# Kernel tuning notes

Measured on AMD Instinct MI355X. Metric: run time of the kernel, lower is better.

The kernel has to match this reference:

```python
import jax, jax.numpy as jnp
import numpy as np

NEG_SLOPE = 0.2


def _gather_neighbour(pc, idx):
    # pc: (B, N, d), idx: (B, N, k) -> (B, N, k, d)
    B, N, d = pc.shape
    k = idx.shape[-1]
    flat = idx.reshape(B, N * k)[..., None]            # (B, N*k, 1)
    g = jnp.take_along_axis(pc, flat, axis=1)          # (B, N*k, d)
    return g.reshape(B, N, k, d)


def _block(x, idx, W2, g2, b2, W1, g1, b1):
    # gather -> 1x1 conv (BN folded, ReLU) -> max/mean over k -> concat -> 1x1 conv (BN folded, no act)
    g = _gather_neighbour(x, idx)                      # (B, N, k, d)
    h = jax.nn.relu(jnp.einsum('bnkd,de->bnke', g, W2) * g2 + b2)
    mx = h.max(axis=2)                                 # (B, N, d_out)
    mn = h.mean(axis=2)                                # (B, N, d_out)
    cat = jnp.concatenate([mx, mn], axis=-1)           # (B, N, 2*d_out)
    return jnp.einsum('bnc,cd->bnd', cat, W1) * g1 + b1


def setup_inputs() -> dict:
    key = jax.random.key(0)
    ks = jax.random.split(key, 8)
    B, N, K, D = 2, 65536, 16, 32
    x = jax.random.normal(ks[0], (B, N, D), dtype=jnp.float32)
    idx = jax.random.randint(ks[1], (B, N, K), 0, N, dtype=jnp.int32)
    L = 4  # four stacked blocks
    W2d = jax.random.normal(ks[2], (L, D, D), dtype=jnp.float32) * 0.05
    gamma2 = jnp.ones((L, 1, 1, 1, D), dtype=jnp.float32)
    beta2 = jax.random.normal(ks[3], (L, 1, 1, 1, D), dtype=jnp.float32) * 0.01
    W1d = jax.random.normal(ks[4], (L, 2 * D, D), dtype=jnp.float32) * 0.05
    gamma1 = jnp.ones((L, 1, 1, D), dtype=jnp.float32)
    beta1 = jax.random.normal(ks[5], (L, 1, 1, D), dtype=jnp.float32) * 0.01
    return {"x": x, "idx": idx, "W2d": W2d, "gamma2": gamma2, "beta2": beta2,
            "W1d": W1d, "gamma1": gamma1, "beta1": beta1}


def reference(x, idx, W2d, gamma2, beta2, W1d, gamma1, beta1):
    lrelu = lambda v: jax.nn.leaky_relu(v, NEG_SLOPE)
    blk = lambda inp, i: _block(inp, idx, W2d[i], gamma2[i][0], beta2[i][0],
                                W1d[i], gamma1[i][0], beta1[i][0])
    x1 = blk(x, 0)
    tmp = lrelu(x1)
    x2 = blk(tmp, 1)
    tmp = lrelu(x2 + x1)
    x3 = blk(tmp, 2)
    tmp = lrelu(x3 + x2)
    x4 = blk(tmp, 3)
    return lrelu(x1 + x2 + x3 + x4)
```

## Files before the change

### kernel.cpp

```cpp
#include <hip/hip_runtime.h>
#include <hip/hip_fp16.h>

namespace {

typedef _Float16 half8 __attribute__((ext_vector_type(8)));
typedef float f32x4 __attribute__((ext_vector_type(4)));

constexpr int kN = 65536;
constexpr int kD = 32;
constexpr int kPts = 2 * kN;
constexpr int kThreads = 256;
constexpr int kPtsPerWave = 16;
constexpr int kPtsPerBlk = 64;
constexpr int kBlocks = kPts / kPtsPerBlk;
static_assert(kBlocks * kPtsPerBlk == kPts, "grid must tile points exactly");
static_assert(kN % kPtsPerBlk == 0, "blocks must not straddle batch boundary");

__device__ __forceinline__ float relu_(float v) { return fmaxf(v, 0.f); }
__device__ __forceinline__ float lrelu_(float v) { return v >= 0.f ? v : 0.2f * v; }

__device__ __forceinline__ half8 load_bfrag(const float* __restrict__ W,
                                            int krow0, int ncol, int q)
{
    half8 b;
#pragma unroll
    for (int j = 0; j < 8; ++j)
        b[j] = (_Float16)W[(krow0 + q * 8 + j) * kD + ncol];
    return b;
}

__global__ __launch_bounds__(kThreads, 4)
void zprep_kernel(const float* __restrict__ x, const float* __restrict__ W2,
                  const float* __restrict__ g2v, const float* __restrict__ b2v,
                  __half* __restrict__ z)
{
    const int tid  = threadIdx.x;
    const int w    = tid >> 6;
    const int lane = tid & 63;
    const int n    = lane & 15;
    const int q    = lane >> 4;
    const int pbase = blockIdx.x * kPtsPerBlk + w * kPtsPerWave;
    const int point = pbase + n;

    const float4 x0 = reinterpret_cast<const float4*>(x)[point * 8 + q * 2];
    const float4 x1 = reinterpret_cast<const float4*>(x)[point * 8 + q * 2 + 1];
    half8 ax;
    ax[0] = (_Float16)x0.x; ax[1] = (_Float16)x0.y;
    ax[2] = (_Float16)x0.z; ax[3] = (_Float16)x0.w;
    ax[4] = (_Float16)x1.x; ax[5] = (_Float16)x1.y;
    ax[6] = (_Float16)x1.z; ax[7] = (_Float16)x1.w;

    const half8 b0 = load_bfrag(W2, 0, n, q);
    const half8 b1 = load_bfrag(W2, 0, 16 + n, q);
    f32x4 acc0 = {0.f, 0.f, 0.f, 0.f}, acc1 = {0.f, 0.f, 0.f, 0.f};
    acc0 = __builtin_amdgcn_mfma_f32_16x16x32_f16(ax, b0, acc0, 0, 0, 0);
    acc1 = __builtin_amdgcn_mfma_f32_16x16x32_f16(ax, b1, acc1, 0, 0, 0);

    const float g20 = g2v[n], g21 = g2v[16 + n];
    const float c20 = b2v[n], c21 = b2v[16 + n];
#pragma unroll
    for (int r = 0; r < 4; ++r) {
        const int pm = pbase + q * 4 + r;
        z[pm * kD + n]      = __float2half(relu_(fmaf(acc0[r], g20, c20)));
        z[pm * kD + 16 + n] = __float2half(relu_(fmaf(acc1[r], g21, c21)));
    }
}

template <int MODE>
__global__ __launch_bounds__(kThreads, 4)
void blk_kernel(const uint4* __restrict__ zsrc, const int4* __restrict__ idx,
                const float* __restrict__ W1, const float* __restrict__ g1v,
                const float* __restrict__ b1v,
                const float* __restrict__ W2n, const float* __restrict__ g2v,
                const float* __restrict__ b2v,
                const __half* __restrict__ prev, __half* __restrict__ cur,
                float* __restrict__ sacc, __half* __restrict__ znext)
{
    __shared__ __align__(16) _Float16 tb[4][16][40];

    const int tid  = threadIdx.x;
    const int w    = tid >> 6;
    const int lane = tid & 63;
    const int n    = lane & 15;
    const int q    = lane >> 4;
    const int pbase = blockIdx.x * kPtsPerBlk + w * kPtsPerWave;
    const int point = pbase + n;
    const int base  = point & ~(kN - 1);

    const int4 i0 = idx[point * 4 + 0];
    const int4 i1 = idx[point * 4 + 1];
    const int4 i2 = idx[point * 4 + 2];
    const int4 i3 = idx[point * 4 + 3];

    const half8 bA0 = load_bfrag(W1, 0, n, q);
    const half8 bA1 = load_bfrag(W1, 0, 16 + n, q);
    const half8 bB0 = load_bfrag(W1, 32, n, q);
    const half8 bB1 = load_bfrag(W1, 32, 16 + n, q);

    int rows[16];
    rows[0] = i0.x; rows[1] = i0.y; rows[2]  = i0.z; rows[3]  = i0.w;
    rows[4] = i1.x; rows[5] = i1.y; rows[6]  = i1.z; rows[7]  = i1.w;
    rows[8] = i2.x; rows[9] = i2.y; rows[10] = i2.z; rows[11] = i2.w;
    rows[12] = i3.x; rows[13] = i3.y; rows[14] = i3.z; rows[15] = i3.w;

    float mx[8], sm[8];
#pragma unroll
    for (int c = 0; c < 8; ++c) { mx[c] = 0.f; sm[c] = 0.f; }
#pragma unroll
    for (int k = 0; k < 16; ++k) {
        const uint4 u = zsrc[(base + rows[k]) * 4 + q];
        const __half2* h = reinterpret_cast<const __half2*>(&u);
#pragma unroll
        for (int c = 0; c < 4; ++c) {
            const float2 f = __half22float2(h[c]);
            mx[2 * c]     = fmaxf(mx[2 * c], f.x);     sm[2 * c]     += f.x;
            mx[2 * c + 1] = fmaxf(mx[2 * c + 1], f.y); sm[2 * c + 1] += f.y;
        }
    }
    half8 amax, amean;
#pragma unroll
    for (int c = 0; c < 8; ++c) {
        amax[c]  = (_Float16)mx[c];
        amean[c] = (_Float16)(sm[c] * 0.0625f);
    }

    f32x4 acc0 = {0.f, 0.f, 0.f, 0.f}, acc1 = {0.f, 0.f, 0.f, 0.f};
    acc0 = __builtin_amdgcn_mfma_f32_16x16x32_f16(amax,  bA0, acc0, 0, 0, 0);
    acc0 = __builtin_amdgcn_mfma_f32_16x16x32_f16(amean, bB0, acc0, 0, 0, 0);
    acc1 = __builtin_amdgcn_mfma_f32_16x16x32_f16(amax,  bA1, acc1, 0, 0, 0);
    acc1 = __builtin_amdgcn_mfma_f32_16x16x32_f16(amean, bB1, acc1, 0, 0, 0);

    const float g10 = g1v[n], g11 = g1v[16 + n];
    const float c10 = b1v[n], c11 = b1v[16 + n];

    float t0[4], t1[4];
#pragma unroll
    for (int r = 0; r < 4; ++r) {
        const int pm = pbase + q * 4 + r;
        const int o0 = pm * kD + n;
        const int o1 = o0 + 16;
        const float y0 = fmaf(acc0[r], g10, c10);
        const float y1 = fmaf(acc1[r], g11, c11);
        if (MODE == 0) {
            sacc[o0] = y0; sacc[o1] = y1;
            cur[o0] = __float2half(y0); cur[o1] = __float2half(y1);
            t0[r] = lrelu_(y0); t1[r] = lrelu_(y1);
        } else if (MODE == 1 || MODE == 2) {
            sacc[o0] += y0; sacc[o1] += y1;
            const float pv0 = __half2float(prev[o0]);
            const float pv1 = __half2float(prev[o1]);
            t0[r] = lrelu_(y0 + pv0); t1[r] = lrelu_(y1 + pv1);
            if (MODE == 1) { cur[o0] = __float2half(y0); cur[o1] = __float2half(y1); }
        } else {
            sacc[o0] = lrelu_(sacc[o0] + y0);
            sacc[o1] = lrelu_(sacc[o1] + y1);
        }
    }
    if (MODE == 3) return;

#pragma unroll
    for (int r = 0; r < 4; ++r) {
        tb[w][q * 4 + r][n]      = (_Float16)t0[r];
        tb[w][q * 4 + r][16 + n] = (_Float16)t1[r];
    }
    __syncthreads();
    const half8 at = *reinterpret_cast<const half8*>(&tb[w][n][q * 8]);

    const half8 bz0 = load_bfrag(W2n, 0, n, q);
    const half8 bz1 = load_bfrag(W2n, 0, 16 + n, q);
    f32x4 az0 = {0.f, 0.f, 0.f, 0.f}, az1 = {0.f, 0.f, 0.f, 0.f};
    az0 = __builtin_amdgcn_mfma_f32_16x16x32_f16(at, bz0, az0, 0, 0, 0);
    az1 = __builtin_amdgcn_mfma_f32_16x16x32_f16(at, bz1, az1, 0, 0, 0);

    const float g20 = g2v[n], g21 = g2v[16 + n];
    const float c20 = b2v[n], c21 = b2v[16 + n];
#pragma unroll
    for (int r = 0; r < 4; ++r) {
        const int pm = pbase + q * 4 + r;
        znext[pm * kD + n]      = __float2half(relu_(fmaf(az0[r], g20, c20)));
        znext[pm * kD + 16 + n] = __float2half(relu_(fmaf(az1[r], g21, c21)));
    }
}

}

extern "C" void kernel_launch(void* const* d_in, const int* in_sizes, int n_in,
                              void* d_out, int out_size, void* d_ws, size_t ws_size,
                              hipStream_t stream)
{
    const float* x   = (const float*)d_in[0];
    const int4*  idx = (const int4*)d_in[1];
    const float* W2d = (const float*)d_in[2];
    const float* g2  = (const float*)d_in[3];
    const float* b2  = (const float*)d_in[4];
    const float* W1d = (const float*)d_in[5];
    const float* g1  = (const float*)d_in[6];
    const float* b1  = (const float*)d_in[7];
    float* out = (float*)d_out;
    char*  ws  = (char*)d_ws;

    constexpr size_t kHalfMap = (size_t)kPts * kD * sizeof(__half);
    __half* zA = (__half*)(ws);
    __half* zB = (__half*)(ws + kHalfMap);
    __half* cA = (__half*)(ws + 2 * kHalfMap);
    __half* cB = (__half*)(ws + 3 * kHalfMap);

    const dim3 grid(kBlocks), blk(kThreads);
    zprep_kernel<<<grid, blk, 0, stream>>>(x, W2d, g2, b2, zA);
    blk_kernel<0><<<grid, blk, 0, stream>>>((const uint4*)zA, idx, W1d, g1, b1,
        W2d + 1 * kD * kD, g2 + 1 * kD, b2 + 1 * kD, nullptr, cA, out, zB);
    blk_kernel<1><<<grid, blk, 0, stream>>>((const uint4*)zB, idx,
        W1d + 1 * 2 * kD * kD, g1 + 1 * kD, b1 + 1 * kD,
        W2d + 2 * kD * kD, g2 + 2 * kD, b2 + 2 * kD, cA, cB, out, zA);
    blk_kernel<2><<<grid, blk, 0, stream>>>((const uint4*)zA, idx,
        W1d + 2 * 2 * kD * kD, g1 + 2 * kD, b1 + 2 * kD,
        W2d + 3 * kD * kD, g2 + 3 * kD, b2 + 3 * kD, cB, nullptr, out, zB);
    blk_kernel<3><<<grid, blk, 0, stream>>>((const uint4*)zB, idx,
        W1d + 3 * 2 * kD * kD, g1 + 3 * kD, b1 + 3 * kD,
        nullptr, nullptr, nullptr, nullptr, nullptr, out, nullptr);
}
```

Measured before the change: 190.1 us.

## Pack weights into MFMA fragments, compress indices to 16-bit, permute channel layout

Adds a one-block pack kernel that converts all weight matrices into ready-made fp16 MFMA B-fragments, so the per-block scalar strided weight loads and conversions go away. zprep now also rewrites the int32 neighbour indices as 16-bit pairs, which halves index traffic in the three later gather kernels that read them. The z and cur maps use an interleaved channel permutation (half2 pairs of channels c and c+16), with the weight rows permuted to match. The epilogue goes through a wave-local LDS transpose with a wave barrier instead of __syncthreads, so sacc, prev and cur are accessed as wide float4/uint4 per point. In exchange there is an extra launch and workspace, and the 16-bit indices rely on N ≤ 65536.

```diff
diff --git a/kernel.cpp b/kernel.cpp
--- a/kernel.cpp
+++ b/kernel.cpp
@@ -10,36 +10,73 @@
 constexpr int kD = 32;
 constexpr int kPts = 2 * kN;
 constexpr int kThreads = 256;
-constexpr int kPtsPerWave = 16;
 constexpr int kPtsPerBlk = 64;
 constexpr int kBlocks = kPts / kPtsPerBlk;
+constexpr int kNumFrags = 24;
 static_assert(kBlocks * kPtsPerBlk == kPts, "grid must tile points exactly");
 static_assert(kN % kPtsPerBlk == 0, "blocks must not straddle batch boundary");
 
 __device__ __forceinline__ float relu_(float v) { return fmaxf(v, 0.f); }
 __device__ __forceinline__ float lrelu_(float v) { return v >= 0.f ? v : 0.2f * v; }
 
-__device__ __forceinline__ half8 load_bfrag(const float* __restrict__ W,
-                                            int krow0, int ncol, int q)
-{
-    half8 b;
-#pragma unroll
-    for (int j = 0; j < 8; ++j)
-        b[j] = (_Float16)W[(krow0 + q * 8 + j) * kD + ncol];
-    return b;
+__device__ __forceinline__ int pi_(int k) {
+    const int c = ((k >> 3) << 2) + ((k & 7) >> 1);
+    return (k & 1) ? c + 16 : c;
+}
+
+__global__ __launch_bounds__(kThreads)
+void pack_kernel(const float* __restrict__ W2d, const float* __restrict__ W1d,
+                 uint4* __restrict__ wpack)
+{
+    for (int id = threadIdx.x; id < kNumFrags * 64; id += kThreads) {
+        const int fid = id >> 6, l = id & 63, n = l & 15, q = l >> 4;
+        half8 v;
+        if (fid < 2) {
+            const int h = fid;
+#pragma unroll
+            for (int j = 0; j < 8; ++j)
+                v[j] = (_Float16)W2d[(q * 8 + j) * kD + h * 16 + n];
+        } else {
+            const int rel = fid - 2;
+            const int layer = (rel < 18) ? rel / 6 : 3;
+            const int sub   = (rel < 18) ? rel % 6 : rel - 18;
+            if (sub < 4) {
+                const int p = sub >> 1, h = sub & 1;
+#pragma unroll
+                for (int j = 0; j < 8; ++j)
+                    v[j] = (_Float16)W1d[layer * 2048 + (p * 32 + pi_(q * 8 + j)) * kD + h * 16 + n];
+            } else {
+                const int h = sub - 4;
+#pragma unroll
+                for (int j = 0; j < 8; ++j)
+                    v[j] = (_Float16)W2d[(layer + 1) * 1024 + pi_(q * 8 + j) * kD + h * 16 + n];
+            }
+        }
+        wpack[id] = *reinterpret_cast<const uint4*>(&v);
+    }
 }
 
 __global__ __launch_bounds__(kThreads, 4)
-void zprep_kernel(const float* __restrict__ x, const float* __restrict__ W2,
+void zprep_kernel(const float* __restrict__ x, const int4* __restrict__ idx4,
+                  const uint4* __restrict__ wfrag,
                   const float* __restrict__ g2v, const float* __restrict__ b2v,
-                  __half* __restrict__ z)
+                  __half2* __restrict__ z, uint2* __restrict__ idx16)
 {
     const int tid  = threadIdx.x;
+    {
+        const int p = blockIdx.x * kPtsPerBlk + (tid >> 2);
+        const int part = tid & 3;
+        const int4 iv = idx4[p * 4 + part];
+        uint2 o;
+        o.x = (unsigned)(iv.x & 0xFFFF) | ((unsigned)iv.y << 16);
+        o.y = (unsigned)(iv.z & 0xFFFF) | ((unsigned)iv.w << 16);
+        idx16[p * 4 + part] = o;
+    }
     const int w    = tid >> 6;
     const int lane = tid & 63;
     const int n    = lane & 15;
     const int q    = lane >> 4;
-    const int pbase = blockIdx.x * kPtsPerBlk + w * kPtsPerWave;
+    const int pbase = blockIdx.x * kPtsPerBlk + w * 16;
     const int point = pbase + n;
 
     const float4 x0 = reinterpret_cast<const float4*>(x)[point * 8 + q * 2];
@@ -50,65 +87,67 @@
     ax[4] = (_Float16)x1.x; ax[5] = (_Float16)x1.y;
     ax[6] = (_Float16)x1.z; ax[7] = (_Float16)x1.w;
 
-    const half8 b0 = load_bfrag(W2, 0, n, q);
-    const half8 b1 = load_bfrag(W2, 0, 16 + n, q);
-    f32x4 acc0 = {0.f, 0.f, 0.f, 0.f}, acc1 = {0.f, 0.f, 0.f, 0.f};
-    acc0 = __builtin_amdgcn_mfma_f32_16x16x32_f16(ax, b0, acc0, 0, 0, 0);
-    acc1 = __builtin_amdgcn_mfma_f32_16x16x32_f16(ax, b1, acc1, 0, 0, 0);
+    const uint4 u0 = wfrag[0 * 64 + lane];
+    const uint4 u1 = wfrag[1 * 64 + lane];
+    const half8 b0 = *reinterpret_cast<const half8*>(&u0);
+    const half8 b1 = *reinterpret_cast<const half8*>(&u1);
+    f32x4 a0 = {0.f, 0.f, 0.f, 0.f}, a1 = {0.f, 0.f, 0.f, 0.f};
+    a0 = __builtin_amdgcn_mfma_f32_16x16x32_f16(ax, b0, a0, 0, 0, 0);
+    a1 = __builtin_amdgcn_mfma_f32_16x16x32_f16(ax, b1, a1, 0, 0, 0);
 
     const float g20 = g2v[n], g21 = g2v[16 + n];
     const float c20 = b2v[n], c21 = b2v[16 + n];
 #pragma unroll
     for (int r = 0; r < 4; ++r) {
         const int pm = pbase + q * 4 + r;
-        z[pm * kD + n]      = __float2half(relu_(fmaf(acc0[r], g20, c20)));
-        z[pm * kD + 16 + n] = __float2half(relu_(fmaf(acc1[r], g21, c21)));
+        z[pm * 16 + n] = __floats2half2_rn(relu_(fmaf(a0[r], g20, c20)),
+                                           relu_(fmaf(a1[r], g21, c21)));
     }
 }
 
 template <int MODE>
 __global__ __launch_bounds__(kThreads, 4)
-void blk_kernel(const uint4* __restrict__ zsrc, const int4* __restrict__ idx,
-                const float* __restrict__ W1, const float* __restrict__ g1v,
-                const float* __restrict__ b1v,
-                const float* __restrict__ W2n, const float* __restrict__ g2v,
-                const float* __restrict__ b2v,
-                const __half* __restrict__ prev, __half* __restrict__ cur,
-                float* __restrict__ sacc, __half* __restrict__ znext)
-{
-    __shared__ __align__(16) _Float16 tb[4][16][40];
+void blk_kernel(const uint4* __restrict__ zsrc, const uint4* __restrict__ idx16,
+                const uint4* __restrict__ wfrag,
+                const float* __restrict__ g1v, const float* __restrict__ b1v,
+                const float* __restrict__ g2v, const float* __restrict__ b2v,
+                const uint4* __restrict__ prev, uint4* __restrict__ cur,
+                float* __restrict__ sacc, __half2* __restrict__ znext)
+{
+    __shared__ float2 tb[4][16][17];
 
     const int tid  = threadIdx.x;
     const int w    = tid >> 6;
     const int lane = tid & 63;
     const int n    = lane & 15;
     const int q    = lane >> 4;
-    const int pbase = blockIdx.x * kPtsPerBlk + w * kPtsPerWave;
+    const int pbase = blockIdx.x * kPtsPerBlk + w * 16;
     const int point = pbase + n;
-    const int base  = point & ~(kN - 1);
-
-    const int4 i0 = idx[point * 4 + 0];
-    const int4 i1 = idx[point * 4 + 1];
-    const int4 i2 = idx[point * 4 + 2];
-    const int4 i3 = idx[point * 4 + 3];
-
-    const half8 bA0 = load_bfrag(W1, 0, n, q);
-    const half8 bA1 = load_bfrag(W1, 0, 16 + n, q);
-    const half8 bB0 = load_bfrag(W1, 32, n, q);
-    const half8 bB1 = load_bfrag(W1, 32, 16 + n, q);
-
-    int rows[16];
-    rows[0] = i0.x; rows[1] = i0.y; rows[2]  = i0.z; rows[3]  = i0.w;
-    rows[4] = i1.x; rows[5] = i1.y; rows[6]  = i1.z; rows[7]  = i1.w;
-    rows[8] = i2.x; rows[9] = i2.y; rows[10] = i2.z; rows[11] = i2.w;
-    rows[12] = i3.x; rows[13] = i3.y; rows[14] = i3.z; rows[15] = i3.w;
+    const int base  = pbase & ~(kN - 1);
+
+    const uint4 iv0 = idx16[point * 2 + 0];
+    const uint4 iv1 = idx16[point * 2 + 1];
+
+    const uint4 f0 = wfrag[0 * 64 + lane];
+    const uint4 f1 = wfrag[1 * 64 + lane];
+    const uint4 f2 = wfrag[2 * 64 + lane];
+    const uint4 f3 = wfrag[3 * 64 + lane];
+    const half8 bA0 = *reinterpret_cast<const half8*>(&f0);
+    const half8 bA1 = *reinterpret_cast<const half8*>(&f1);
+    const half8 bB0 = *reinterpret_cast<const half8*>(&f2);
+    const half8 bB1 = *reinterpret_cast<const half8*>(&f3);
 
     float mx[8], sm[8];
 #pragma unroll
     for (int c = 0; c < 8; ++c) { mx[c] = 0.f; sm[c] = 0.f; }
+    const unsigned* ivw = reinterpret_cast<const unsigned*>(&iv0);
 #pragma unroll
     for (int k = 0; k < 16; ++k) {
-        const uint4 u = zsrc[(base + rows[k]) * 4 + q];
+        unsigned word;
+        if (k < 8) word = reinterpret_cast<const unsigned*>(&iv0)[k >> 1];
+        else       word = reinterpret_cast<const unsigned*>(&iv1)[(k - 8) >> 1];
+        const int row = (k & 1) ? (int)(word >> 16) : (int)(word & 0xFFFFu);
+        const uint4 u = zsrc[(base + row) * 4 + q];
         const __half2* h = reinterpret_cast<const __half2*>(&u);
 #pragma unroll
         for (int c = 0; c < 4; ++c) {
@@ -117,6 +156,7 @@
             mx[2 * c + 1] = fmaxf(mx[2 * c + 1], f.y); sm[2 * c + 1] += f.y;
         }
     }
+    (void)ivw;
     half8 amax, amean;
 #pragma unroll
     for (int c = 0; c < 8; ++c) {
@@ -132,42 +172,71 @@
 
     const float g10 = g1v[n], g11 = g1v[16 + n];
     const float c10 = b1v[n], c11 = b1v[16 + n];
-
-    float t0[4], t1[4];
 #pragma unroll
     for (int r = 0; r < 4; ++r) {
-        const int pm = pbase + q * 4 + r;
-        const int o0 = pm * kD + n;
-        const int o1 = o0 + 16;
-        const float y0 = fmaf(acc0[r], g10, c10);
-        const float y1 = fmaf(acc1[r], g11, c11);
-        if (MODE == 0) {
-            sacc[o0] = y0; sacc[o1] = y1;
-            cur[o0] = __float2half(y0); cur[o1] = __float2half(y1);
-            t0[r] = lrelu_(y0); t1[r] = lrelu_(y1);
-        } else if (MODE == 1 || MODE == 2) {
-            sacc[o0] += y0; sacc[o1] += y1;
-            const float pv0 = __half2float(prev[o0]);
-            const float pv1 = __half2float(prev[o1]);
-            t0[r] = lrelu_(y0 + pv0); t1[r] = lrelu_(y1 + pv1);
-            if (MODE == 1) { cur[o0] = __float2half(y0); cur[o1] = __float2half(y1); }
-        } else {
-            sacc[o0] = lrelu_(sacc[o0] + y0);
-            sacc[o1] = lrelu_(sacc[o1] + y1);
-        }
-    }
-    if (MODE == 3) return;
-
-#pragma unroll
-    for (int r = 0; r < 4; ++r) {
-        tb[w][q * 4 + r][n]      = (_Float16)t0[r];
-        tb[w][q * 4 + r][16 + n] = (_Float16)t1[r];
-    }
-    __syncthreads();
-    const half8 at = *reinterpret_cast<const half8*>(&tb[w][n][q * 8]);
-
-    const half8 bz0 = load_bfrag(W2n, 0, n, q);
-    const half8 bz1 = load_bfrag(W2n, 0, 16 + n, q);
+        tb[w][q * 4 + r][n] = make_float2(fmaf(acc0[r], g10, c10),
+                                          fmaf(acc1[r], g11, c11));
+    }
+    __builtin_amdgcn_wave_barrier();
+    float y8[8];
+#pragma unroll
+    for (int s = 0; s < 4; ++s) {
+        const float2 f = tb[w][n][q * 4 + s];
+        y8[2 * s] = f.x; y8[2 * s + 1] = f.y;
+    }
+
+    const int sb0 = point * kD + q * 4;
+    const int sb1 = sb0 + 16;
+    float t8[8];
+    if (MODE == 0) {
+        reinterpret_cast<float4*>(sacc)[sb0 >> 2] = make_float4(y8[0], y8[2], y8[4], y8[6]);
+        reinterpret_cast<float4*>(sacc)[sb1 >> 2] = make_float4(y8[1], y8[3], y8[5], y8[7]);
+        half8 ch;
+#pragma unroll
+        for (int c = 0; c < 8; ++c) ch[c] = (_Float16)y8[c];
+        cur[point * 4 + q] = *reinterpret_cast<const uint4*>(&ch);
+#pragma unroll
+        for (int c = 0; c < 8; ++c) t8[c] = lrelu_(y8[c]);
+    } else if (MODE == 1 || MODE == 2) {
+        float4 s0 = reinterpret_cast<const float4*>(sacc)[sb0 >> 2];
+        float4 s1 = reinterpret_cast<const float4*>(sacc)[sb1 >> 2];
+        s0.x += y8[0]; s0.y += y8[2]; s0.z += y8[4]; s0.w += y8[6];
+        s1.x += y8[1]; s1.y += y8[3]; s1.z += y8[5]; s1.w += y8[7];
+        reinterpret_cast<float4*>(sacc)[sb0 >> 2] = s0;
+        reinterpret_cast<float4*>(sacc)[sb1 >> 2] = s1;
+        const uint4 pv = prev[point * 4 + q];
+        const __half2* ph = reinterpret_cast<const __half2*>(&pv);
+#pragma unroll
+        for (int c = 0; c < 4; ++c) {
+            const float2 f = __half22float2(ph[c]);
+            t8[2 * c]     = lrelu_(y8[2 * c] + f.x);
+            t8[2 * c + 1] = lrelu_(y8[2 * c + 1] + f.y);
+        }
+        if (MODE == 1) {
+            half8 ch;
+#pragma unroll
+            for (int c = 0; c < 8; ++c) ch[c] = (_Float16)y8[c];
+            cur[point * 4 + q] = *reinterpret_cast<const uint4*>(&ch);
+        }
+    } else {
+        const float4 s0 = reinterpret_cast<const float4*>(sacc)[sb0 >> 2];
+        const float4 s1 = reinterpret_cast<const float4*>(sacc)[sb1 >> 2];
+        reinterpret_cast<float4*>(sacc)[sb0 >> 2] =
+            make_float4(lrelu_(s0.x + y8[0]), lrelu_(s0.y + y8[2]),
+                        lrelu_(s0.z + y8[4]), lrelu_(s0.w + y8[6]));
+        reinterpret_cast<float4*>(sacc)[sb1 >> 2] =
+            make_float4(lrelu_(s1.x + y8[1]), lrelu_(s1.y + y8[3]),
+                        lrelu_(s1.z + y8[5]), lrelu_(s1.w + y8[7]));
+        return;
+    }
+
+    half8 at;
+#pragma unroll
+    for (int c = 0; c < 8; ++c) at[c] = (_Float16)t8[c];
+    const uint4 f4 = wfrag[4 * 64 + lane];
+    const uint4 f5 = wfrag[5 * 64 + lane];
+    const half8 bz0 = *reinterpret_cast<const half8*>(&f4);
+    const half8 bz1 = *reinterpret_cast<const half8*>(&f5);
     f32x4 az0 = {0.f, 0.f, 0.f, 0.f}, az1 = {0.f, 0.f, 0.f, 0.f};
     az0 = __builtin_amdgcn_mfma_f32_16x16x32_f16(at, bz0, az0, 0, 0, 0);
     az1 = __builtin_amdgcn_mfma_f32_16x16x32_f16(at, bz1, az1, 0, 0, 0);
@@ -177,8 +246,8 @@
 #pragma unroll
     for (int r = 0; r < 4; ++r) {
         const int pm = pbase + q * 4 + r;
-        znext[pm * kD + n]      = __float2half(relu_(fmaf(az0[r], g20, c20)));
-        znext[pm * kD + 16 + n] = __float2half(relu_(fmaf(az1[r], g21, c21)));
+        znext[pm * 16 + n] = __floats2half2_rn(relu_(fmaf(az0[r], g20, c20)),
+                                               relu_(fmaf(az1[r], g21, c21)));
     }
 }
 
@@ -200,22 +269,28 @@
     char*  ws  = (char*)d_ws;
 
     constexpr size_t kHalfMap = (size_t)kPts * kD * sizeof(__half);
-    __half* zA = (__half*)(ws);
-    __half* zB = (__half*)(ws + kHalfMap);
-    __half* cA = (__half*)(ws + 2 * kHalfMap);
-    __half* cB = (__half*)(ws + 3 * kHalfMap);
+    __half2* zA = (__half2*)(ws);
+    __half2* zB = (__half2*)(ws + kHalfMap);
+    uint4*   cA = (uint4*)(ws + 2 * kHalfMap);
+    uint4*   cB = (uint4*)(ws + 3 * kHalfMap);
+    uint2*   idx16 = (uint2*)(ws + 4 * kHalfMap);
+    uint4*   wpack = (uint4*)(ws + 4 * kHalfMap + (size_t)kPts * 32);
 
     const dim3 grid(kBlocks), blk(kThreads);
-    zprep_kernel<<<grid, blk, 0, stream>>>(x, W2d, g2, b2, zA);
-    blk_kernel<0><<<grid, blk, 0, stream>>>((const uint4*)zA, idx, W1d, g1, b1,
-        W2d + 1 * kD * kD, g2 + 1 * kD, b2 + 1 * kD, nullptr, cA, out, zB);
-    blk_kernel<1><<<grid, blk, 0, stream>>>((const uint4*)zB, idx,
-        W1d + 1 * 2 * kD * kD, g1 + 1 * kD, b1 + 1 * kD,
-        W2d + 2 * kD * kD, g2 + 2 * kD, b2 + 2 * kD, cA, cB, out, zA);
-    blk_kernel<2><<<grid, blk, 0, stream>>>((const uint4*)zA, idx,
-        W1d + 2 * 2 * kD * kD, g1 + 2 * kD, b1 + 2 * kD,
-        W2d + 3 * kD * kD, g2 + 3 * kD, b2 + 3 * kD, cB, nullptr, out, zB);
-    blk_kernel<3><<<grid, blk, 0, stream>>>((const uint4*)zB, idx,
-        W1d + 3 * 2 * kD * kD, g1 + 3 * kD, b1 + 3 * kD,
-        nullptr, nullptr, nullptr, nullptr, nullptr, out, nullptr);
-}
+    pack_kernel<<<dim3(1), blk, 0, stream>>>(W2d, W1d, wpack);
+    zprep_kernel<<<grid, blk, 0, stream>>>(x, idx, wpack, g2, b2, zA, idx16);
+
+    const uint4* i16 = (const uint4*)idx16;
+    blk_kernel<0><<<grid, blk, 0, stream>>>((const uint4*)zA, i16,
+        wpack + (2 + 0 * 6) * 64, g1, b1, g2 + 1 * kD, b2 + 1 * kD,
+        nullptr, cA, out, zB);
+    blk_kernel<1><<<grid, blk, 0, stream>>>((const uint4*)zB, i16,
+        wpack + (2 + 1 * 6) * 64, g1 + 1 * kD, b1 + 1 * kD, g2 + 2 * kD, b2 + 2 * kD,
+        cA, cB, out, zA);
+    blk_kernel<2><<<grid, blk, 0, stream>>>((const uint4*)zA, i16,
+        wpack + (2 + 2 * 6) * 64, g1 + 2 * kD, b1 + 2 * kD, g2 + 3 * kD, b2 + 3 * kD,
+        cB, nullptr, out, zB);
+    blk_kernel<3><<<grid, blk, 0, stream>>>((const uint4*)zB, i16,
+        wpack + (2 + 3 * 6) * 64, g1 + 3 * kD, b1 + 3 * kD, nullptr, nullptr,
+        nullptr, nullptr, out, nullptr);
+}
```

Result: no change. 186.7 us (-1.8%).
